# Kernel tuning notes

Hardware: AMD Instinct MI355X
Metric: run time of the kernel (lower is better)

## Reference

```python
import jax, jax.numpy as jnp
import numpy as np

B, BOND, N, ATOM, UNITS = 256, 5, 128, 64, 128


def setup_inputs() -> dict:
    key = jax.random.key(0)
    k1, k2, k3 = jax.random.split(key, 3)
    adjacency = jax.random.uniform(k1, (B, BOND, N, N), dtype=jnp.float32)
    features = jax.random.normal(k2, (B, N, ATOM), dtype=jnp.float32)
    # per-sample unique kernel: (global_batch, bond_dim, atom_dim, units)
    kernel = jax.random.normal(k3, (B, BOND, ATOM, UNITS), dtype=jnp.float32) * 0.05
    return {"adjacency": adjacency, "features": features, "kernel": kernel}


def reference(adjacency, features, kernel):
    # aggregate neighbors per bond type: [B, bond, N, atom]
    x = jnp.einsum('bemn,bnd->bemd', adjacency, features)
    # per-sample, per-bond linear transform: [B, bond, N, units]
    x = jnp.einsum('bemd,bedu->bemu', x, kernel)
    # reduce over bond types, then activation: [B, N, units]
    return jax.nn.relu(jnp.sum(x, axis=1))
```

## Files before the change

### kernel.cpp

```cpp
#include <hip/hip_runtime.h>


typedef __attribute__((ext_vector_type(8))) short s8v;
typedef __attribute__((ext_vector_type(4))) float f4v;

__device__ __forceinline__ short f2bf(float f) {
    unsigned u = __builtin_bit_cast(unsigned, f);
    u += 0x7FFFu + ((u >> 16) & 1u);
    return (short)(u >> 16);
}

__device__ __forceinline__ void lds_barrier() {
    asm volatile("s_waitcnt lgkmcnt(0)" ::: "memory");
    __builtin_amdgcn_s_barrier();
    __builtin_amdgcn_sched_barrier(0);
}

__global__ __launch_bounds__(1024, 4)
void rgc_kernel(const float* __restrict__ adj,
                const float* __restrict__ feat,
                const float* __restrict__ ker,
                float* __restrict__ out)
{
    __shared__ __align__(16) short featB[16 * 512];
    __shared__ __align__(16) short kerB[5][16 * 512];
    __shared__ __align__(16) short YA[16][2 * 512];

    const int tid  = threadIdx.x;
    const int w    = tid >> 6;
    const int lane = tid & 63;
    const int c16  = lane & 15;
    const int quad = lane >> 4;
    const int g    = w >> 1;
    const int h    = w & 1;

    const int b = blockIdx.x;
    const float* adjB = adj  + (size_t)b * (5 * 128 * 128);
    const float* feG  = feat + (size_t)b * (128 * 64);
    const float* keG  = ker  + (size_t)b * (5 * 64 * 128);
    float*       outB = out  + (size_t)b * (128 * 128);

    f4v a0[4], a1[4];
    {
        const float* ap = adjB + (16 * g + c16) * 128 + 8 * quad;
        #pragma unroll
        for (int k16 = 0; k16 < 4; ++k16) {
            a0[k16] = *(const f4v*)(ap + 32 * k16);
            a1[k16] = *(const f4v*)(ap + 32 * k16 + 4);
        }
    }

    const int fd  = tid & 63;
    const int fn0 = (tid >> 6) * 8;
    const int ku  = tid & 127;
    const int kd0 = (tid >> 7) * 8;
    const int kerB_off = (ku >> 4) * 1024 + (kd0 >> 5) * 512 + ((kd0 >> 3) & 3) * 128 + (ku & 15) * 8;

    float fv[8];
    #pragma unroll
    for (int j = 0; j < 8; ++j)
        fv[j] = feG[(fn0 + j) * 64 + fd];

    float kv[5][8];
    #pragma unroll
    for (int e = 0; e < 5; ++e)
        #pragma unroll
        for (int j = 0; j < 8; ++j)
            kv[e][j] = keG[e * (64 * 128) + (kd0 + j) * 128 + ku];

    {
        s8v v;
        #pragma unroll
        for (int j = 0; j < 8; ++j) v[j] = f2bf(fv[j]);
        *(s8v*)&featB[((fd >> 4) * 4 + (fn0 >> 5)) * 512 + ((fn0 >> 3) & 3) * 128 + (fd & 15) * 8] = v;
    }
    #pragma unroll
    for (int e = 0; e < 5; ++e) {
        s8v v;
        #pragma unroll
        for (int j = 0; j < 8; ++j) v[j] = f2bf(kv[e][j]);
        *(s8v*)&kerB[e][kerB_off] = v;
    }
    lds_barrier();

    f4v oacc[4] = {};

    for (int e = 0; e < 5; ++e) {
        s8v af[4];
        #pragma unroll
        for (int k16 = 0; k16 < 4; ++k16) {
            #pragma unroll
            for (int j = 0; j < 4; ++j) {
                af[k16][j]     = f2bf(a0[k16][j]);
                af[k16][4 + j] = f2bf(a1[k16][j]);
            }
        }

        if (e < 4) {
            const float* ap = adjB + (e + 1) * (128 * 128) + (16 * g + c16) * 128 + 8 * quad;
            #pragma unroll
            for (int k16 = 0; k16 < 4; ++k16) {
                a0[k16] = *(const f4v*)(ap + 32 * k16);
                a1[k16] = *(const f4v*)(ap + 32 * k16 + 4);
            }
            __builtin_amdgcn_sched_barrier(0);
        }

        f4v yacc[4] = {};
        #pragma unroll
        for (int k16 = 0; k16 < 4; ++k16)
            #pragma unroll
            for (int d16 = 0; d16 < 4; ++d16) {
                s8v bf = *(const s8v*)&featB[(d16 * 4 + k16) * 512 + lane * 8];
                yacc[d16] = __builtin_amdgcn_mfma_f32_16x16x32_bf16(af[k16], bf, yacc[d16], 0, 0, 0);
            }

        #pragma unroll
        for (int d16 = 0; d16 < 4; ++d16) {
            const int base = (d16 >> 1) * 512 + ((2 * d16 + (c16 >> 3)) & 3) * 128 + (c16 & 7);
            #pragma unroll
            for (int r = 0; r < 4; ++r)
                YA[w][base + (4 * quad + r) * 8] = f2bf(yacc[d16][r]);
        }

        {
            s8v afr0 = *(const s8v*)&YA[w][lane * 8];
            s8v afr1 = *(const s8v*)&YA[w][512 + lane * 8];
            #pragma unroll
            for (int n = 0; n < 4; ++n) {
                const int u16 = 4 * h + n;
                s8v b0 = *(const s8v*)&kerB[e][(u16 * 2 + 0) * 512 + lane * 8];
                s8v b1 = *(const s8v*)&kerB[e][(u16 * 2 + 1) * 512 + lane * 8];
                oacc[n] = __builtin_amdgcn_mfma_f32_16x16x32_bf16(afr0, b0, oacc[n], 0, 0, 0);
                oacc[n] = __builtin_amdgcn_mfma_f32_16x16x32_bf16(afr1, b1, oacc[n], 0, 0, 0);
            }
        }
    }

    #pragma unroll
    for (int n = 0; n < 4; ++n)
        #pragma unroll
        for (int r = 0; r < 4; ++r)
            outB[(16 * g + 4 * quad + r) * 128 + 16 * (4 * h + n) + c16] = fmaxf(oacc[n][r], 0.f);
}

extern "C" void kernel_launch(void* const* d_in, const int* in_sizes, int n_in,
                              void* d_out, int out_size, void* d_ws, size_t ws_size,
                              hipStream_t stream)
{
    const float* adj  = (const float*)d_in[0];
    const float* feat = (const float*)d_in[1];
    const float* ker  = (const float*)d_in[2];
    rgc_kernel<<<256, 1024, 0, stream>>>(adj, feat, ker, (float*)d_out);
}
```

Measured before the change: 171.0 us.

## Reassociate to precompute features×kernel per bond and multiply adjacency by it

Computes W_e = features·kernel_e per bond with MFMA into a double-buffered LDS tile, then accumulates adjacency_e·W_e directly into the output. This removes the intermediate per-warp Y transpose and bf16 round-trip through LDS after the adjacency product. It costs more MFMA work, since the adjacency product now has width 128 instead of 64, and it adds a block-wide barrier per bond step to hand off the W buffers.

```diff
diff --git a/kernel.cpp b/kernel.cpp
--- a/kernel.cpp
+++ b/kernel.cpp
@@ -2,6 +2,7 @@
 
 
 typedef __attribute__((ext_vector_type(8))) short s8v;
+typedef __attribute__((ext_vector_type(4))) short s4v;
 typedef __attribute__((ext_vector_type(4))) float f4v;
 
 __device__ __forceinline__ short f2bf(float f) {
@@ -22,9 +23,9 @@
                 const float* __restrict__ ker,
                 float* __restrict__ out)
 {
-    __shared__ __align__(16) short featB[16 * 512];
+    __shared__ __align__(16) short featA[16 * 512];
     __shared__ __align__(16) short kerB[5][16 * 512];
-    __shared__ __align__(16) short YA[16][2 * 512];
+    __shared__ __align__(16) short WB[2][32 * 512];
 
     const int tid  = threadIdx.x;
     const int w    = tid >> 6;
@@ -50,36 +51,57 @@
         }
     }
 
-    const int fd  = tid & 63;
-    const int fn0 = (tid >> 6) * 8;
+    {
+        const float* fp = feG + (16 * (w >> 1) + c16) * 64 + 32 * (w & 1) + 8 * quad;
+        f4v f0 = *(const f4v*)(fp);
+        f4v f1 = *(const f4v*)(fp + 4);
+        s8v v;
+        #pragma unroll
+        for (int j = 0; j < 4; ++j) { v[j] = f2bf(f0[j]); v[4 + j] = f2bf(f1[j]); }
+        *(s8v*)&featA[w * 512 + lane * 8] = v;
+    }
+
     const int ku  = tid & 127;
     const int kd0 = (tid >> 7) * 8;
     const int kerB_off = (ku >> 4) * 1024 + (kd0 >> 5) * 512 + ((kd0 >> 3) & 3) * 128 + (ku & 15) * 8;
+    {
+        float kv[5][8];
+        #pragma unroll
+        for (int e = 0; e < 5; ++e)
+            #pragma unroll
+            for (int j = 0; j < 8; ++j)
+                kv[e][j] = keG[e * (64 * 128) + (kd0 + j) * 128 + ku];
+        #pragma unroll
+        for (int e = 0; e < 5; ++e) {
+            s8v v;
+            #pragma unroll
+            for (int j = 0; j < 8; ++j) v[j] = f2bf(kv[e][j]);
+            *(s8v*)&kerB[e][kerB_off] = v;
+        }
+    }
+    lds_barrier();
 
-    float fv[8];
-    #pragma unroll
-    for (int j = 0; j < 8; ++j)
-        fv[j] = feG[(fn0 + j) * 64 + fd];
-
-    float kv[5][8];
-    #pragma unroll
-    for (int e = 0; e < 5; ++e)
-        #pragma unroll
-        for (int j = 0; j < 8; ++j)
-            kv[e][j] = keG[e * (64 * 128) + (kd0 + j) * 128 + ku];
+    const int wk16 = g >> 1;
+    const int wqt  = 2 * (g & 1) + (quad >> 1);
+    const int wj0  = 4 * (quad & 1);
+    const int wbase = (wqt * 16 + c16) * 8 + wj0;
 
     {
-        s8v v;
+        s8v fa0 = *(const s8v*)&featA[(g * 2 + 0) * 512 + lane * 8];
+        s8v fa1 = *(const s8v*)&featA[(g * 2 + 1) * 512 + lane * 8];
         #pragma unroll
-        for (int j = 0; j < 8; ++j) v[j] = f2bf(fv[j]);
-        *(s8v*)&featB[((fd >> 4) * 4 + (fn0 >> 5)) * 512 + ((fn0 >> 3) & 3) * 128 + (fd & 15) * 8] = v;
-    }
-    #pragma unroll
-    for (int e = 0; e < 5; ++e) {
-        s8v v;
-        #pragma unroll
-        for (int j = 0; j < 8; ++j) v[j] = f2bf(kv[e][j]);
-        *(s8v*)&kerB[e][kerB_off] = v;
+        for (int t = 0; t < 4; ++t) {
+            const int u16 = 4 * h + t;
+            s8v kb0 = *(const s8v*)&kerB[0][(u16 * 2 + 0) * 512 + lane * 8];
+            s8v kb1 = *(const s8v*)&kerB[0][(u16 * 2 + 1) * 512 + lane * 8];
+            f4v wacc = {};
+            wacc = __builtin_amdgcn_mfma_f32_16x16x32_bf16(fa0, kb0, wacc, 0, 0, 0);
+            wacc = __builtin_amdgcn_mfma_f32_16x16x32_bf16(fa1, kb1, wacc, 0, 0, 0);
+            s4v pv;
+            #pragma unroll
+            for (int r = 0; r < 4; ++r) pv[r] = f2bf(wacc[r]);
+            *(s4v*)&WB[0][(u16 * 4 + wk16) * 512 + wbase] = pv;
+        }
     }
     lds_barrier();
 
@@ -104,37 +126,35 @@
                 a1[k16] = *(const f4v*)(ap + 32 * k16 + 4);
             }
             __builtin_amdgcn_sched_barrier(0);
+
+            s8v fa0 = *(const s8v*)&featA[(g * 2 + 0) * 512 + lane * 8];
+            s8v fa1 = *(const s8v*)&featA[(g * 2 + 1) * 512 + lane * 8];
+            #pragma unroll
+            for (int t = 0; t < 4; ++t) {
+                const int u16 = 4 * h + t;
+                s8v kb0 = *(const s8v*)&kerB[e + 1][(u16 * 2 + 0) * 512 + lane * 8];
+                s8v kb1 = *(const s8v*)&kerB[e + 1][(u16 * 2 + 1) * 512 + lane * 8];
+                f4v wacc = {};
+                wacc = __builtin_amdgcn_mfma_f32_16x16x32_bf16(fa0, kb0, wacc, 0, 0, 0);
+                wacc = __builtin_amdgcn_mfma_f32_16x16x32_bf16(fa1, kb1, wacc, 0, 0, 0);
+                s4v pv;
+                #pragma unroll
+                for (int r = 0; r < 4; ++r) pv[r] = f2bf(wacc[r]);
+                *(s4v*)&WB[(e + 1) & 1][(u16 * 4 + wk16) * 512 + wbase] = pv;
+            }
         }
 
-        f4v yacc[4] = {};
         #pragma unroll
-        for (int k16 = 0; k16 < 4; ++k16)
+        for (int n = 0; n < 4; ++n) {
+            const int u16 = 4 * h + n;
             #pragma unroll
-            for (int d16 = 0; d16 < 4; ++d16) {
-                s8v bf = *(const s8v*)&featB[(d16 * 4 + k16) * 512 + lane * 8];
-                yacc[d16] = __builtin_amdgcn_mfma_f32_16x16x32_bf16(af[k16], bf, yacc[d16], 0, 0, 0);
+            for (int k16 = 0; k16 < 4; ++k16) {
+                s8v bfr = *(const s8v*)&WB[e & 1][(u16 * 4 + k16) * 512 + lane * 8];
+                oacc[n] = __builtin_amdgcn_mfma_f32_16x16x32_bf16(af[k16], bfr, oacc[n], 0, 0, 0);
             }
-
-        #pragma unroll
-        for (int d16 = 0; d16 < 4; ++d16) {
-            const int base = (d16 >> 1) * 512 + ((2 * d16 + (c16 >> 3)) & 3) * 128 + (c16 & 7);
-            #pragma unroll
-            for (int r = 0; r < 4; ++r)
-                YA[w][base + (4 * quad + r) * 8] = f2bf(yacc[d16][r]);
         }
 
-        {
-            s8v afr0 = *(const s8v*)&YA[w][lane * 8];
-            s8v afr1 = *(const s8v*)&YA[w][512 + lane * 8];
-            #pragma unroll
-            for (int n = 0; n < 4; ++n) {
-                const int u16 = 4 * h + n;
-                s8v b0 = *(const s8v*)&kerB[e][(u16 * 2 + 0) * 512 + lane * 8];
-                s8v b1 = *(const s8v*)&kerB[e][(u16 * 2 + 1) * 512 + lane * 8];
-                oacc[n] = __builtin_amdgcn_mfma_f32_16x16x32_bf16(afr0, b0, oacc[n], 0, 0, 0);
-                oacc[n] = __builtin_amdgcn_mfma_f32_16x16x32_bf16(afr1, b1, oacc[n], 0, 0, 0);
-            }
-        }
+        if (e < 4) lds_barrier();
     }
 
     #pragma unroll
```

Result: no change. 170.2 us (-0.5%).
